# Performance work log

Hardware: AMD Instinct MI355X
Metric: run time of the kernel (lower is better)

The kernel has to match this reference:

```python
import jax, jax.numpy as jnp
import numpy as np

B, S, E = 2, 2048, 1024
H = 32
DK = E // H  # 32, must equal H for the bilinear einsum to type-check
FFN = 4096
EPS = 1e-5


def layer_norm(x, g, b):
    m = jnp.mean(x, axis=-1, keepdims=True)
    v = jnp.mean((x - m) ** 2, axis=-1, keepdims=True)
    return (x - m) * jax.lax.rsqrt(v + EPS) * g + b


def setup_inputs() -> dict:
    key = jax.random.key(0)
    ks = jax.random.split(key, 16)
    sc = lambda fan_in: 1.0 / np.sqrt(fan_in)
    return {
        "x": jax.random.normal(ks[0], (B, S, E), jnp.float32),
        "Wq": jax.random.normal(ks[1], (E, E), jnp.float32) * sc(E),
        "bq": jax.random.normal(ks[2], (E,), jnp.float32) * 0.02,
        "Wk": jax.random.normal(ks[3], (E, E), jnp.float32) * sc(E),
        "bk": jax.random.normal(ks[4], (E,), jnp.float32) * 0.02,
        "Wv": jax.random.normal(ks[5], (E, E), jnp.float32) * sc(E),
        "bv": jax.random.normal(ks[6], (E,), jnp.float32) * 0.02,
        "kernelW": jax.random.normal(ks[7], (DK, H), jnp.float32),
        "Wo": jax.random.normal(ks[8], (E, E), jnp.float32) * sc(E),
        "bo": jax.random.normal(ks[9], (E,), jnp.float32) * 0.02,
        "W1": jax.random.normal(ks[10], (E, FFN), jnp.float32) * sc(E),
        "b1": jax.random.normal(ks[11], (FFN,), jnp.float32) * 0.02,
        "W2": jax.random.normal(ks[12], (FFN, E), jnp.float32) * sc(FFN),
        "b2": jax.random.normal(ks[13], (E,), jnp.float32) * 0.02,
        "g1": jnp.ones((E,), jnp.float32),
        "beta1": jnp.zeros((E,), jnp.float32),
        "g2": jnp.ones((E,), jnp.float32),
        "beta2": jnp.zeros((E,), jnp.float32),
    }


def reference(x, Wq, bq, Wk, bk, Wv, bv, kernelW, Wo, bo, W1, b1, W2, b2, g1, beta1, g2, beta2):
    # projections -> [B, H, S, DK]
    split = lambda t: t.reshape(B, S, H, DK).transpose(0, 2, 1, 3)
    q = split(x @ Wq + bq)
    k = split(x @ Wk + bk)
    v = split(x @ Wv + bv)
    # bilinear quantum-kernel score: sim[b,h,i,j] = sum_d q[b,h,i,d]*W[d,h]*k[b,h,j,d]
    sim = jnp.einsum('bhqd,dh,bhkd->bhqk', q, kernelW, k)
    attn = jax.nn.softmax(sim, axis=-1)  # dropout is identity at eval
    out = jnp.matmul(attn, v)  # [B, H, S, DK]
    out = out.transpose(0, 2, 1, 3).reshape(B, S, E) @ Wo + bo
    x = layer_norm(x + out, g1, beta1)
    ffn = jax.nn.relu(x @ W1 + b1) @ W2 + b2
    return layer_norm(x + ffn, g2, beta2)
```

## Files before the change

kernel.cpp:

```cpp
#include <hip/hip_runtime.h>


typedef unsigned short u16;
typedef unsigned int u32;
typedef __bf16 bf16x8 __attribute__((ext_vector_type(8)));
typedef float f32x4 __attribute__((ext_vector_type(4)));
typedef float f32x16 __attribute__((ext_vector_type(16)));

__device__ __forceinline__ u16 f2b(float f) {
  union { float f; unsigned u; } x; x.f = f;
  unsigned r = x.u + 0x7FFFu + ((x.u >> 16) & 1u);
  return (u16)(r >> 16);
}

__device__ __forceinline__ unsigned pkbf(float lo, float hi) {
  unsigned r;
  asm("v_cvt_pk_bf16_f32 %0, %1, %2" : "=v"(r) : "v"(lo), "v"(hi));
  return r;
}

__device__ __forceinline__ float expo2(float x) {
#if __has_builtin(__builtin_amdgcn_exp2f)
  return __builtin_amdgcn_exp2f(x);
#else
  return exp2f(x);
#endif
}

#define GLDS16(gp, lp)                                                         \
  __builtin_amdgcn_global_load_lds(                                            \
      (const __attribute__((address_space(1))) void*)(gp),                     \
      (__attribute__((address_space(3))) void*)(lp), 16, 0, 0)

__global__ __launch_bounds__(256) void transpose_cast(
    const float* __restrict__ W, u16* __restrict__ WT, int K, int N) {
  __shared__ float tile[32][33];
  const int tx = threadIdx.x & 31, ty = threadIdx.x >> 5;
  const int n0 = blockIdx.x * 32, k0 = blockIdx.y * 32;
#pragma unroll
  for (int i = 0; i < 4; ++i)
    tile[ty + 8 * i][tx] = W[(size_t)(k0 + ty + 8 * i) * N + n0 + tx];
  __syncthreads();
#pragma unroll
  for (int i = 0; i < 4; ++i)
    WT[(size_t)(n0 + ty + 8 * i) * K + k0 + tx] = f2b(tile[tx][ty + 8 * i]);
}

__global__ __launch_bounds__(256) void cast_b(const float* __restrict__ x,
                                              u16* __restrict__ y) {
  int i = blockIdx.x * 256 + threadIdx.x;
  float4 v = ((const float4*)x)[i];
  ushort4 o;
  o.x = f2b(v.x); o.y = f2b(v.y); o.z = f2b(v.z); o.w = f2b(v.w);
  ((ushort4*)y)[i] = o;
}

template <int MODE, int BN>
__global__ __launch_bounds__(256) void gemmT(
    const u16* __restrict__ A, const u16* __restrict__ BT,
    const float* __restrict__ bias, const float* __restrict__ bias2,
    const float* __restrict__ bias3, const float* __restrict__ res,
    void* __restrict__ outp, const float* __restrict__ kW, int N_, int K_) {
  constexpr int ABYT = 128 * 32 * 2;
  constexpr int BBYT = BN * 32 * 2;
  constexpr int STRIDE = ABYT + BBYT;
  constexpr int MI = (BN == 128) ? 4 : 2;
  __shared__ __align__(16) char SH[2 * STRIDE];
  const int t = threadIdx.x, lane = t & 63, wid = t >> 6;
  const int gx = gridDim.x;
  const int id = blockIdx.y * gx + blockIdx.x;
  const int nb = gx * gridDim.y;
  const int sid = (id & 7) * (nb >> 3) + (id >> 3);
  const int bx = sid % gx;
  int by = sid / gx;
  int kh6 = 0;
  if constexpr (MODE == 6) { kh6 = by >> 5; by &= 31; }
  const int m0 = by * 128, n0 = bx * BN;
  const int wr = (BN == 128) ? (wid >> 1) * 64 : wid * 32;
  const int wc = (BN == 128) ? (wid & 1) * 64 : 0;
  const int lr = lane & 15, lg = lane >> 4;
  const int K = K_;
  const int koff = (MODE == 6) ? kh6 * 2048 : 0;

  f32x4 acc[MI][4] = {};

  const u16* ga0 = A + (size_t)(m0 + (t >> 2)) * K + koff + (t & 3) * 8;
  const u16* ga1 = ga0 + (size_t)64 * K;
  const u16* gb0 = BT + (size_t)(n0 + (t >> 2)) * K + koff + (t & 3) * 8;
  const u16* gb1 = gb0 + (size_t)64 * K;
  const int stA = wid * 1024;

#define STAGE(CUR, KT)                                                         \
  {                                                                            \
    char* l_ = (char*)SH + (CUR) * STRIDE + stA;                               \
    const size_t o_ = (size_t)(KT) * 32;                                       \
    GLDS16(ga0 + o_, l_);                                                      \
    GLDS16(ga1 + o_, l_ + 4096);                                               \
    GLDS16(gb0 + o_, l_ + ABYT);                                               \
    if constexpr (BN == 128) GLDS16(gb1 + o_, l_ + ABYT + 4096);               \
  }

  const int nk = (MODE == 6) ? 64 : (K >> 5);
  STAGE(0, 0);
  __syncthreads();
  int cur = 0;
  for (int kt = 0; kt < nk; ++kt) {
    if (kt + 1 < nk) STAGE(cur ^ 1, kt + 1);
    const char* l = (const char*)SH + cur * STRIDE;
    bf16x8 af[MI], bf[4];
#pragma unroll
    for (int i = 0; i < MI; ++i)
      af[i] = *(const bf16x8*)(l + (wr + i * 16 + lr) * 64 + lg * 16);
#pragma unroll
    for (int i = 0; i < 4; ++i)
      bf[i] = *(const bf16x8*)(l + ABYT + (wc + i * 16 + lr) * 64 + lg * 16);
#pragma unroll
    for (int mi = 0; mi < MI; ++mi)
#pragma unroll
      for (int ni = 0; ni < 4; ++ni)
        acc[mi][ni] = __builtin_amdgcn_mfma_f32_16x16x32_bf16(
            af[mi], bf[ni], acc[mi][ni], 0, 0, 0);
    __syncthreads();
    cur ^= 1;
  }
#undef STAGE

#pragma unroll
  for (int mi = 0; mi < MI; ++mi) {
#pragma unroll
    for (int ni = 0; ni < 4; ++ni) {
      const int row = m0 + wr + mi * 16 + lg * 4;
      const int col = n0 + wc + ni * 16 + lr;
      f32x4 v = acc[mi][ni];
      if constexpr (MODE == 2) {
        const float bv = bias[col];
        float* o = (float*)outp;
#pragma unroll
        for (int r = 0; r < 4; ++r) {
          const int rr = row + r;
          o[(size_t)rr * N_ + col] = v[r] + bv + res[(size_t)rr * N_ + col];
        }
      } else if constexpr (MODE == 3) {
        const float bv = bias[col];
        u16* o = (u16*)outp;
#pragma unroll
        for (int r = 0; r < 4; ++r) {
          const int rr = row + r;
          float y = v[r] + bv;
          o[(size_t)rr * N_ + col] = f2b(y > 0.f ? y : 0.f);
        }
      } else if constexpr (MODE == 6) {
        float* o = (kh6 == 0) ? (float*)outp : (float*)res;
#pragma unroll
        for (int r = 0; r < 4; ++r) {
          const int rr = row + r;
          o[(size_t)rr * N_ + col] = v[r];
        }
      } else {
        const int proj = col >> 10, c = col & 1023;
        const int h = c >> 5, d = c & 31;
        u16* qout = (u16*)outp;
        if (proj == 0) {
          const float bv = bias[c];
          const float sc = kW[d * 32 + h] * 1.44269504089f;
#pragma unroll
          for (int r = 0; r < 4; ++r) {
            const int rr = row + r;
            const int bb = rr >> 11, s = rr & 2047;
            qout[(size_t)(((bb * 32 + h) * 2048) + s) * 32 + d] =
                f2b((v[r] + bv) * sc);
          }
        } else if (proj == 1) {
          const float bv = bias2[c];
          u16* kout = qout + 4194304;
          const int c2 = d >> 3;
#pragma unroll
          for (int r = 0; r < 4; ++r) {
            const int rr = row + r;
            const int bb = rr >> 11, s = rr & 2047;
            const int k = s & 63;
            const int g = ((k >> 5) << 1) | (c2 >> 1);
            kout[(size_t)(bb * 32 + h) * 65536 + (s >> 6) * 2048 + g * 512 +
                 (c2 & 1) * 256 + (k & 31) * 8 + (d & 7)] = f2b(v[r] + bv);
          }
        } else {
          const float bv = bias3[c];
          u16* vout = qout + 8388608;
          const int bb = row >> 11, s0 = row & 2047;
          const int k = s0 & 63;
          const int cc = k >> 3, rb = cc >> 1, hb = cc & 1, e = k & 7;
          ushort4 st;
          st.x = f2b(v[0] + bv); st.y = f2b(v[1] + bv);
          st.z = f2b(v[2] + bv); st.w = f2b(v[3] + bv);
          *(ushort4*)(vout + (size_t)(bb * 32 + h) * 65536 +
                      (s0 >> 6) * 2048 + rb * 512 + hb * 256 + d * 8 + e) = st;
        }
      }
    }
  }
}

__device__ __forceinline__ void attn_tile(
    const bf16x8& k0, const bf16x8& k1, const bf16x8& k2, const bf16x8& k3,
    const bf16x8& v0, const bf16x8& v1, const bf16x8& v2, const bf16x8& v3,
    const bf16x8& qb0, const bf16x8& qb1,
    f32x16& acc, float& la, float& lb, float& lc, float& ld) {
  const f32x16 z16 = {};
  f32x16 s0 = __builtin_amdgcn_mfma_f32_32x32x16_bf16(k0, qb0, z16, 0, 0, 0);
  s0 = __builtin_amdgcn_mfma_f32_32x32x16_bf16(k1, qb1, s0, 0, 0, 0);
  f32x16 s1 = __builtin_amdgcn_mfma_f32_32x32x16_bf16(k2, qb0, z16, 0, 0, 0);
  s1 = __builtin_amdgcn_mfma_f32_32x32x16_bf16(k3, qb1, s1, 0, 0, 0);
  float p0[16], p1[16];
#pragma unroll
  for (int r = 0; r < 16; ++r) p0[r] = expo2(s0[r]);
#pragma unroll
  for (int r = 0; r < 16; ++r) p1[r] = expo2(s1[r]);
#pragma unroll
  for (int r = 0; r < 4; ++r) {
    la += p0[r] + p1[r];
    lb += p0[4 + r] + p1[4 + r];
    lc += p0[8 + r] + p1[8 + r];
    ld += p0[12 + r] + p1[12 + r];
  }
  {
    u32 x0 = pkbf(p0[0], p0[1]), x1 = pkbf(p0[2], p0[3]);
    u32 y0 = pkbf(p0[4], p0[5]), y1 = pkbf(p0[6], p0[7]);
    asm("v_permlane32_swap_b32 %0, %1" : "+v"(x0), "+v"(y0));
    asm("v_permlane32_swap_b32 %0, %1" : "+v"(x1), "+v"(y1));
    union { u32 d[4]; bf16x8 v; } u;
    u.d[0] = x0; u.d[1] = x1; u.d[2] = y0; u.d[3] = y1;
    acc = __builtin_amdgcn_mfma_f32_32x32x16_bf16(v0, u.v, acc, 0, 0, 0);
  }
  {
    u32 x0 = pkbf(p0[8], p0[9]), x1 = pkbf(p0[10], p0[11]);
    u32 y0 = pkbf(p0[12], p0[13]), y1 = pkbf(p0[14], p0[15]);
    asm("v_permlane32_swap_b32 %0, %1" : "+v"(x0), "+v"(y0));
    asm("v_permlane32_swap_b32 %0, %1" : "+v"(x1), "+v"(y1));
    union { u32 d[4]; bf16x8 v; } u;
    u.d[0] = x0; u.d[1] = x1; u.d[2] = y0; u.d[3] = y1;
    acc = __builtin_amdgcn_mfma_f32_32x32x16_bf16(v1, u.v, acc, 0, 0, 0);
  }
  {
    u32 x0 = pkbf(p1[0], p1[1]), x1 = pkbf(p1[2], p1[3]);
    u32 y0 = pkbf(p1[4], p1[5]), y1 = pkbf(p1[6], p1[7]);
    asm("v_permlane32_swap_b32 %0, %1" : "+v"(x0), "+v"(y0));
    asm("v_permlane32_swap_b32 %0, %1" : "+v"(x1), "+v"(y1));
    union { u32 d[4]; bf16x8 v; } u;
    u.d[0] = x0; u.d[1] = x1; u.d[2] = y0; u.d[3] = y1;
    acc = __builtin_amdgcn_mfma_f32_32x32x16_bf16(v2, u.v, acc, 0, 0, 0);
  }
  {
    u32 x0 = pkbf(p1[8], p1[9]), x1 = pkbf(p1[10], p1[11]);
    u32 y0 = pkbf(p1[12], p1[13]), y1 = pkbf(p1[14], p1[15]);
    asm("v_permlane32_swap_b32 %0, %1" : "+v"(x0), "+v"(y0));
    asm("v_permlane32_swap_b32 %0, %1" : "+v"(x1), "+v"(y1));
    union { u32 d[4]; bf16x8 v; } u;
    u.d[0] = x0; u.d[1] = x1; u.d[2] = y0; u.d[3] = y1;
    acc = __builtin_amdgcn_mfma_f32_32x32x16_bf16(v3, u.v, acc, 0, 0, 0);
  }
}

__global__ __launch_bounds__(512) void attn_kernel(
    const u16* __restrict__ Q, const u16* __restrict__ K,
    const u16* __restrict__ VT, u16* __restrict__ O) {
  __shared__ __align__(16) char LDSB[32768];
  const int t = threadIdx.x, wid = t >> 6, lane = t & 63;
  const int qg = wid & 3, kh = wid >> 2;
  const int bid = blockIdx.x;
  const int swz = (bid & 7) * 128 + (bid >> 3);
  const int bh = swz >> 4;
  const int qt = swz & 15;
  const int q0 = qt * 128 + qg * 32;
  const int lq = lane & 31, hi = lane >> 5;
  const u16* Qh = Q + (size_t)bh * 65536;
  const u16* Kh = K + (size_t)bh * 65536;
  const u16* Vh = VT + (size_t)bh * 65536;

  const bf16x8 qb0 = *(const bf16x8*)(Qh + (size_t)(q0 + lq) * 32 + hi * 8);
  const bf16x8 qb1 = *(const bf16x8*)(Qh + (size_t)(q0 + lq) * 32 + 16 + hi * 8);

  const u16* kg = Kh + wid * 512 + lane * 8;
  const u16* vg = Vh + wid * 512 + lane * 8;
  const int lds_w = wid * 1024;

#define STAGEA(CUR, I)                                                         \
  if (wid < 4) {                                                               \
    char* b_ = LDSB + (CUR) * 16384 + lds_w;                                   \
    GLDS16(kg + (size_t)(I) * 2048, b_);                                       \
    GLDS16(vg + (size_t)(I) * 2048, b_ + 4096);                                \
    GLDS16(kg + (size_t)(16 + (I)) * 2048, b_ + 8192);                         \
    GLDS16(vg + (size_t)(16 + (I)) * 2048, b_ + 12288);                        \
  }

  f32x16 acc = {};
  float la = 0.f, lb = 0.f, lc = 0.f, ld = 0.f;

  STAGEA(0, 0);
  __syncthreads();
  int cur = 0;
#pragma unroll 1
  for (int i = 0; i < 16; ++i) {
    if (i < 15) STAGEA(cur ^ 1, i + 1);
    const char* kb = LDSB + cur * 16384 + kh * 8192 + lane * 16;
    const bf16x8 ka0 = *(const bf16x8*)(kb);
    const bf16x8 ka1 = *(const bf16x8*)(kb + 1024);
    const bf16x8 ka2 = *(const bf16x8*)(kb + 2048);
    const bf16x8 ka3 = *(const bf16x8*)(kb + 3072);
    const bf16x8 va0 = *(const bf16x8*)(kb + 4096);
    const bf16x8 va1 = *(const bf16x8*)(kb + 5120);
    const bf16x8 va2 = *(const bf16x8*)(kb + 6144);
    const bf16x8 va3 = *(const bf16x8*)(kb + 7168);
    attn_tile(ka0, ka1, ka2, ka3, va0, va1, va2, va3, qb0, qb1,
              acc, la, lb, lc, ld);
    __syncthreads();
    cur ^= 1;
  }
#undef STAGEA

  float lrun = (la + lb) + (lc + ld);
  lrun += __shfl_xor(lrun, 32);

  float* sm_acc = (float*)LDSB;
  float* sm_l = (float*)(LDSB + 16384);
  if (kh == 1) {
    sm_l[qg * 32 + lq] = lrun;
#pragma unroll
    for (int r = 0; r < 16; ++r) sm_acc[(qg * 64 + lane) * 16 + r] = acc[r];
  }
  __syncthreads();
  if (kh == 0) {
    const float inv = 1.f / (lrun + sm_l[qg * 32 + lq]);
    const int bb = bh >> 5, h = bh & 31;
    u16* o = O + (size_t)(bb * 2048 + q0 + lq) * 1024 + h * 32;
#pragma unroll
    for (int g = 0; g < 4; ++g) {
      ushort4 st;
      st.x = f2b((acc[g * 4 + 0] + sm_acc[(qg * 64 + lane) * 16 + g * 4 + 0]) * inv);
      st.y = f2b((acc[g * 4 + 1] + sm_acc[(qg * 64 + lane) * 16 + g * 4 + 1]) * inv);
      st.z = f2b((acc[g * 4 + 2] + sm_acc[(qg * 64 + lane) * 16 + g * 4 + 2]) * inv);
      st.w = f2b((acc[g * 4 + 3] + sm_acc[(qg * 64 + lane) * 16 + g * 4 + 3]) * inv);
      *(ushort4*)(o + g * 8 + hi * 4) = st;
    }
  }
}

template <int WB>
__global__ __launch_bounds__(256) void ln_kernel(
    const float* X, const float* __restrict__ g, const float* __restrict__ b,
    float* outf, u16* __restrict__ outb) {
  const int wid = threadIdx.x >> 6, lane = threadIdx.x & 63;
  const int row = blockIdx.x * 4 + wid;
  const float4* X4 = (const float4*)(X + (size_t)row * 1024);
  float4 xs[4];
  float s = 0.f, sq = 0.f;
#pragma unroll
  for (int i = 0; i < 4; ++i) {
    xs[i] = X4[lane + i * 64];
    s += xs[i].x + xs[i].y + xs[i].z + xs[i].w;
    sq += xs[i].x * xs[i].x + xs[i].y * xs[i].y + xs[i].z * xs[i].z + xs[i].w * xs[i].w;
  }
#pragma unroll
  for (int m = 1; m < 64; m <<= 1) { s += __shfl_xor(s, m); sq += __shfl_xor(sq, m); }
  const float mean = s * (1.f / 1024.f);
  float var = sq * (1.f / 1024.f) - mean * mean;
  var = var > 0.f ? var : 0.f;
  const float rstd = rsqrtf(var + 1e-5f);
  const float4* g4 = (const float4*)g;
  const float4* b4 = (const float4*)b;
  float4* of = (float4*)(outf + (size_t)row * 1024);
#pragma unroll
  for (int i = 0; i < 4; ++i) {
    const int c = lane + i * 64;
    const float4 gv = g4[c], bv = b4[c], x = xs[i];
    float4 y;
    y.x = (x.x - mean) * rstd * gv.x + bv.x;
    y.y = (x.y - mean) * rstd * gv.y + bv.y;
    y.z = (x.z - mean) * rstd * gv.z + bv.z;
    y.w = (x.w - mean) * rstd * gv.w + bv.w;
    of[c] = y;
    if constexpr (WB) {
      ushort4 yb;
      yb.x = f2b(y.x); yb.y = f2b(y.y); yb.z = f2b(y.z); yb.w = f2b(y.w);
      ((ushort4*)(outb + (size_t)row * 1024))[c] = yb;
    }
  }
}

__global__ __launch_bounds__(256) void ln2sum_kernel(
    const float* __restrict__ PA, const float* __restrict__ PB,
    const float* __restrict__ R, const float* __restrict__ bias,
    const float* __restrict__ g, const float* __restrict__ b,
    float* __restrict__ out) {
  const int wid = threadIdx.x >> 6, lane = threadIdx.x & 63;
  const int row = blockIdx.x * 4 + wid;
  const float4* A4 = (const float4*)(PA + (size_t)row * 1024);
  const float4* B4 = (const float4*)(PB + (size_t)row * 1024);
  const float4* R4 = (const float4*)(R + (size_t)row * 1024);
  const float4* Bi4 = (const float4*)bias;
  float4 xs[4];
  float s = 0.f, sq = 0.f;
#pragma unroll
  for (int i = 0; i < 4; ++i) {
    const int c = lane + i * 64;
    const float4 a = A4[c], pb = B4[c], r = R4[c], bi = Bi4[c];
    float4 x;
    x.x = a.x + pb.x + r.x + bi.x;
    x.y = a.y + pb.y + r.y + bi.y;
    x.z = a.z + pb.z + r.z + bi.z;
    x.w = a.w + pb.w + r.w + bi.w;
    xs[i] = x;
    s += x.x + x.y + x.z + x.w;
    sq += x.x * x.x + x.y * x.y + x.z * x.z + x.w * x.w;
  }
#pragma unroll
  for (int m = 1; m < 64; m <<= 1) { s += __shfl_xor(s, m); sq += __shfl_xor(sq, m); }
  const float mean = s * (1.f / 1024.f);
  float var = sq * (1.f / 1024.f) - mean * mean;
  var = var > 0.f ? var : 0.f;
  const float rstd = rsqrtf(var + 1e-5f);
  const float4* g4 = (const float4*)g;
  const float4* b4 = (const float4*)b;
  float4* of = (float4*)(out + (size_t)row * 1024);
#pragma unroll
  for (int i = 0; i < 4; ++i) {
    const int c = lane + i * 64;
    const float4 gv = g4[c], bv = b4[c], x = xs[i];
    float4 y;
    y.x = (x.x - mean) * rstd * gv.x + bv.x;
    y.y = (x.y - mean) * rstd * gv.y + bv.y;
    y.z = (x.z - mean) * rstd * gv.z + bv.z;
    y.w = (x.w - mean) * rstd * gv.w + bv.w;
    of[c] = y;
  }
}

extern "C" void kernel_launch(void* const* d_in, const int* in_sizes, int n_in,
                              void* d_out, int out_size, void* d_ws,
                              size_t ws_size, hipStream_t stream) {
  const float* x   = (const float*)d_in[0];
  const float* Wq  = (const float*)d_in[1];
  const float* bq  = (const float*)d_in[2];
  const float* Wk  = (const float*)d_in[3];
  const float* bk  = (const float*)d_in[4];
  const float* Wv  = (const float*)d_in[5];
  const float* bv  = (const float*)d_in[6];
  const float* kW  = (const float*)d_in[7];
  const float* Wo  = (const float*)d_in[8];
  const float* bo  = (const float*)d_in[9];
  const float* W1  = (const float*)d_in[10];
  const float* b1  = (const float*)d_in[11];
  const float* W2  = (const float*)d_in[12];
  const float* b2  = (const float*)d_in[13];
  const float* g1  = (const float*)d_in[14];
  const float* be1 = (const float*)d_in[15];
  const float* g2  = (const float*)d_in[16];
  const float* be2 = (const float*)d_in[17];

  char* ws = (char*)d_ws;
  const size_t MB = 1024 * 1024;
  u16*   WqT = (u16*)(ws + 0 * MB);
  u16*   WoT = (u16*)(ws + 6 * MB);
  u16*   W1T = (u16*)(ws + 8 * MB);
  u16*   W2T = (u16*)(ws + 16 * MB);
  float* r1  = (float*)(ws + 24 * MB);
  u16*   xb  = (u16*)(ws + 40 * MB);
  u16*   qhB = (u16*)(ws + 48 * MB);
  u16*   khB = (u16*)(ws + 56 * MB);
  u16*   vTB = (u16*)(ws + 64 * MB);
  u16*   hf  = (u16*)(ws + 40 * MB);
  u16*   ao  = (u16*)(ws + 72 * MB);
  u16*   x1b = (u16*)(ws + 80 * MB);
  float* r2a = (float*)(ws + 0 * MB);
  float* r2b = (float*)(ws + 72 * MB);

  const dim3 blk(256);

  transpose_cast<<<dim3(32, 32), blk, 0, stream>>>(Wq, WqT, 1024, 1024);
  transpose_cast<<<dim3(32, 32), blk, 0, stream>>>(Wk, WqT + 1048576, 1024, 1024);
  transpose_cast<<<dim3(32, 32), blk, 0, stream>>>(Wv, WqT + 2097152, 1024, 1024);
  transpose_cast<<<dim3(32, 32), blk, 0, stream>>>(Wo, WoT, 1024, 1024);
  transpose_cast<<<dim3(128, 32), blk, 0, stream>>>(W1, W1T, 1024, 4096);
  transpose_cast<<<dim3(32, 128), blk, 0, stream>>>(W2, W2T, 4096, 1024);
  cast_b<<<4096, blk, 0, stream>>>(x, xb);

  gemmT<5, 128><<<dim3(24, 32), blk, 0, stream>>>(
      xb, WqT, bq, bk, bv, nullptr, qhB, kW, 3072, 1024);

  attn_kernel<<<1024, dim3(512), 0, stream>>>(qhB, khB, vTB, ao);

  gemmT<2, 64><<<dim3(16, 32), blk, 0, stream>>>(
      ao, WoT, bo, nullptr, nullptr, x, r1, nullptr, 1024, 1024);
  ln_kernel<1><<<1024, blk, 0, stream>>>(r1, g1, be1, r1, x1b);
  gemmT<3, 128><<<dim3(32, 32), blk, 0, stream>>>(
      x1b, W1T, b1, nullptr, nullptr, nullptr, hf, nullptr, 4096, 1024);
  gemmT<6, 64><<<dim3(16, 64), blk, 0, stream>>>(
      hf, W2T, nullptr, nullptr, nullptr, r2b, r2a, nullptr, 1024, 4096);
  ln2sum_kernel<<<1024, blk, 0, stream>>>(r2a, r2b, r1, b2, g2, be2,
                                          (float*)d_out);

  (void)in_sizes; (void)n_in; (void)out_size; (void)ws_size;
}
```

Before: 258.6 us.

## Split FFN2 GEMM four ways along K with bf16 partials and wider tiles

The second FFN GEMM now splits K into four 1024-wide slices instead of two, switches to 128-wide N tiles, and writes bf16 partial sums instead of fp32. The final layernorm kernel reads and sums the four bf16 partials. The aim is to keep the same 1024-block parallelism with larger, more reuse-friendly tiles while halving the bytes of each partial. Rounding partial sums to bf16 adds precision error before the residual add.

```diff
diff --git a/kernel.cpp b/kernel.cpp
--- a/kernel.cpp
+++ b/kernel.cpp
@@ -11,6 +11,10 @@
   union { float f; unsigned u; } x; x.f = f;
   unsigned r = x.u + 0x7FFFu + ((x.u >> 16) & 1u);
   return (u16)(r >> 16);
+}
+
+__device__ __forceinline__ float b2f(u16 u) {
+  union { u32 u; float f; } x; x.u = (u32)u << 16; return x.f;
 }
 
 __device__ __forceinline__ unsigned pkbf(float lo, float hi) {
@@ -80,7 +84,7 @@
   const int wc = (BN == 128) ? (wid & 1) * 64 : 0;
   const int lr = lane & 15, lg = lane >> 4;
   const int K = K_;
-  const int koff = (MODE == 6) ? kh6 * 2048 : 0;
+  const int koff = (MODE == 6) ? kh6 * 1024 : 0;
 
   f32x4 acc[MI][4] = {};
 
@@ -100,7 +104,7 @@
     if constexpr (BN == 128) GLDS16(gb1 + o_, l_ + ABYT + 4096);               \
   }
 
-  const int nk = (MODE == 6) ? 64 : (K >> 5);
+  const int nk = (MODE == 6) ? 32 : (K >> 5);
   STAGE(0, 0);
   __syncthreads();
   int cur = 0;
@@ -150,11 +154,12 @@
           o[(size_t)rr * N_ + col] = f2b(y > 0.f ? y : 0.f);
         }
       } else if constexpr (MODE == 6) {
-        float* o = (kh6 == 0) ? (float*)outp : (float*)res;
+        u16* o = (kh6 < 2) ? ((u16*)outp + (size_t)kh6 * 4194304)
+                           : ((u16*)res + (size_t)(kh6 - 2) * 4194304);
 #pragma unroll
         for (int r = 0; r < 4; ++r) {
           const int rr = row + r;
-          o[(size_t)rr * N_ + col] = v[r];
+          o[(size_t)rr * N_ + col] = f2b(v[r]);
         }
       } else {
         const int proj = col >> 10, c = col & 1023;
@@ -387,14 +392,17 @@
 }
 
 __global__ __launch_bounds__(256) void ln2sum_kernel(
-    const float* __restrict__ PA, const float* __restrict__ PB,
+    const u16* __restrict__ P0, const u16* __restrict__ P1,
+    const u16* __restrict__ P2, const u16* __restrict__ P3,
     const float* __restrict__ R, const float* __restrict__ bias,
     const float* __restrict__ g, const float* __restrict__ b,
     float* __restrict__ out) {
   const int wid = threadIdx.x >> 6, lane = threadIdx.x & 63;
   const int row = blockIdx.x * 4 + wid;
-  const float4* A4 = (const float4*)(PA + (size_t)row * 1024);
-  const float4* B4 = (const float4*)(PB + (size_t)row * 1024);
+  const ushort4* A4 = (const ushort4*)(P0 + (size_t)row * 1024);
+  const ushort4* B4 = (const ushort4*)(P1 + (size_t)row * 1024);
+  const ushort4* C4 = (const ushort4*)(P2 + (size_t)row * 1024);
+  const ushort4* D4 = (const ushort4*)(P3 + (size_t)row * 1024);
   const float4* R4 = (const float4*)(R + (size_t)row * 1024);
   const float4* Bi4 = (const float4*)bias;
   float4 xs[4];
@@ -402,12 +410,13 @@
 #pragma unroll
   for (int i = 0; i < 4; ++i) {
     const int c = lane + i * 64;
-    const float4 a = A4[c], pb = B4[c], r = R4[c], bi = Bi4[c];
+    const ushort4 a = A4[c], pb = B4[c], pc = C4[c], pd = D4[c];
+    const float4 r = R4[c], bi = Bi4[c];
     float4 x;
-    x.x = a.x + pb.x + r.x + bi.x;
-    x.y = a.y + pb.y + r.y + bi.y;
-    x.z = a.z + pb.z + r.z + bi.z;
-    x.w = a.w + pb.w + r.w + bi.w;
+    x.x = (b2f(a.x) + b2f(pb.x)) + (b2f(pc.x) + b2f(pd.x)) + r.x + bi.x;
+    x.y = (b2f(a.y) + b2f(pb.y)) + (b2f(pc.y) + b2f(pd.y)) + r.y + bi.y;
+    x.z = (b2f(a.z) + b2f(pb.z)) + (b2f(pc.z) + b2f(pd.z)) + r.z + bi.z;
+    x.w = (b2f(a.w) + b2f(pb.w)) + (b2f(pc.w) + b2f(pd.w)) + r.w + bi.w;
     xs[i] = x;
     s += x.x + x.y + x.z + x.w;
     sq += x.x * x.x + x.y * x.y + x.z * x.z + x.w * x.w;
@@ -470,8 +479,8 @@
   u16*   hf  = (u16*)(ws + 40 * MB);
   u16*   ao  = (u16*)(ws + 72 * MB);
   u16*   x1b = (u16*)(ws + 80 * MB);
-  float* r2a = (float*)(ws + 0 * MB);
-  float* r2b = (float*)(ws + 72 * MB);
+  u16*   p0  = (u16*)(ws + 0 * MB);
+  u16*   p2  = (u16*)(ws + 72 * MB);
 
   const dim3 blk(256);
 
@@ -493,10 +502,11 @@
   ln_kernel<1><<<1024, blk, 0, stream>>>(r1, g1, be1, r1, x1b);
   gemmT<3, 128><<<dim3(32, 32), blk, 0, stream>>>(
       x1b, W1T, b1, nullptr, nullptr, nullptr, hf, nullptr, 4096, 1024);
-  gemmT<6, 64><<<dim3(16, 64), blk, 0, stream>>>(
-      hf, W2T, nullptr, nullptr, nullptr, r2b, r2a, nullptr, 1024, 4096);
-  ln2sum_kernel<<<1024, blk, 0, stream>>>(r2a, r2b, r1, b2, g2, be2,
-                                          (float*)d_out);
+  gemmT<6, 128><<<dim3(8, 128), blk, 0, stream>>>(
+      hf, W2T, nullptr, nullptr, nullptr, (const float*)p2, p0, nullptr,
+      1024, 4096);
+  ln2sum_kernel<<<1024, blk, 0, stream>>>(p0, p0 + 4194304, p2, p2 + 4194304,
+                                          r1, b2, g2, be2, (float*)d_out);
 
   (void)in_sizes; (void)n_in; (void)out_size; (void)ws_size;
 }
```

After: 253.5 us. -2.0%, faster.
